# Kernel optimization log

Measured on AMD Instinct MI355X. Metric: run time of the kernel, lower is better.

The kernel has to match this reference:

```python
import jax, jax.numpy as jnp
import numpy as np

N, E, G, D, H = 50000, 800000, 64, 64, 256  # nodes, edges, graphs, feat dim, mlp hidden


def _mlp(x, W1, b1, W2, b2):
    return jax.nn.relu(x @ W1 + b1) @ W2 + b2


def _param(key, fan_in, fan_out):
    return jax.random.normal(key, (fan_in, fan_out), dtype=jnp.float32) * (1.0 / np.sqrt(fan_in))


def setup_inputs() -> dict:
    key = jax.random.key(0)
    ks = jax.random.split(key, 16)
    inp = {
        "nf": jax.random.normal(ks[0], (N, D), dtype=jnp.float32),
        "ef": jax.random.normal(ks[1], (E, D), dtype=jnp.float32),
        "u": jax.random.normal(ks[2], (G, D), dtype=jnp.float32),
        "src": jax.random.randint(ks[3], (E,), 0, N, dtype=jnp.int32),
        "dst": jax.random.randint(ks[4], (E,), 0, N, dtype=jnp.int32),
        "node_gid": jnp.sort(jax.random.randint(ks[5], (N,), 0, G, dtype=jnp.int32)),
        "edge_gid": jnp.sort(jax.random.randint(ks[6], (E,), 0, G, dtype=jnp.int32)),
        # edge_model: in = De + 2*Dn + Du = 4D
        "eW1": _param(ks[7], 4 * D, H), "eb1": jnp.zeros((H,), jnp.float32),
        "eW2": _param(ks[8], H, D),     "eb2": jnp.zeros((D,), jnp.float32),
        # node_model: in = De + Dn + Du = 3D
        "nW1": _param(ks[9], 3 * D, H), "nb1": jnp.zeros((H,), jnp.float32),
        "nW2": _param(ks[10], H, D),    "nb2": jnp.zeros((D,), jnp.float32),
        # global_model: in = De + Dn + Du = 3D
        "gW1": _param(ks[11], 3 * D, H), "gb1": jnp.zeros((H,), jnp.float32),
        "gW2": _param(ks[12], H, D),     "gb2": jnp.zeros((D,), jnp.float32),
    }
    return inp


def reference(nf, ef, u, src, dst, node_gid, edge_gid,
              eW1, eb1, eW2, eb2, nW1, nb1, nW2, nb2, gW1, gb1, gW2, gb2):
    # --- edge update: cat([ef, src_nf, dst_nf, u_per_edge]) -> edge MLP ---
    u_e = u[edge_gid]                                   # [E, D] (repeat_interleave by batch_num_edges)
    em_in = jnp.concatenate([ef, nf[src], nf[dst], u_e], axis=-1)  # [E, 4D]
    ef_new = _mlp(em_in, eW1, eb1, eW2, eb2)            # [E, D]

    # --- message = copy_e, reduce = sum at destination nodes ---
    agg_m = jax.ops.segment_sum(ef_new, dst, num_segments=N)       # [N, D]

    # --- node update: cat([agg_m, nf, u_per_node]) -> node MLP ---
    u_n = u[node_gid]                                   # [N, D]
    nm_in = jnp.concatenate([agg_m, nf, u_n], axis=-1)  # [N, 3D]
    nf_new = _mlp(nm_in, nW1, nb1, nW2, nb2)            # [N, D]

    # --- global update: per-graph sum readouts of updated edge/node feats ---
    e_aggr = jax.ops.segment_sum(ef_new, edge_gid, num_segments=G)  # [G, D]
    n_aggr = jax.ops.segment_sum(nf_new, node_gid, num_segments=G)  # [G, D]
    gm_in = jnp.concatenate([e_aggr, n_aggr, u], axis=-1)           # [G, 3D]
    u_new = _mlp(gm_in, gW1, gb1, gW2, gb2)             # [G, D]

    return nf_new, ef_new, u_new
```

## Files before the change

kernel.cpp:

```cpp
#include <hip/hip_runtime.h>
#include <stdint.h>
#include <stddef.h>

#define NN 50000
#define EE 800000
#define GG 64
#define DD 64
#define HH 256

typedef float f32x4 __attribute__((ext_vector_type(4)));
typedef short s16x8 __attribute__((ext_vector_type(8)));
typedef short s16x4 __attribute__((ext_vector_type(4)));

__device__ __forceinline__ short f2bf(float f) {
    union { float f; unsigned u; } v; v.f = f;
    return (short)((v.u + 0x7FFFu + ((v.u >> 16) & 1u)) >> 16);
}

__device__ __forceinline__ s16x4 f2bf4(f32x4 v) {
    s16x4 h = { f2bf(v.x), f2bf(v.y), f2bf(v.z), f2bf(v.w) };
    return h;
}

__global__ void prep_weights(const float* __restrict__ eW1, const float* __restrict__ eW2,
                             const float* __restrict__ nW1, const float* __restrict__ nW2,
                             short* __restrict__ W1t, short* __restrict__ W2t,
                             short* __restrict__ NW1t, short* __restrict__ NW2t) {
    int idx = blockIdx.x * blockDim.x + threadIdx.x;
    {
        int n = idx >> 8, k = idx & 255;
        W1t[idx] = f2bf(eW1[k * 256 + n]);
    }
    if (idx < 49152) {
        int n = idx / 192, k = idx - n * 192;
        NW1t[idx] = f2bf(nW1[k * 256 + n]);
    }
    if (idx < 16384) {
        int n = idx >> 8, k = idx & 255;
        W2t[idx]  = f2bf(eW2[k * 64 + n]);
        NW2t[idx] = f2bf(nW2[k * 64 + n]);
    }
}

#define SA1 264
#define SAN 200

__global__ __launch_bounds__(256, 2) void edge_kernel(
    const float* __restrict__ nf, const float* __restrict__ ef, const float* __restrict__ u,
    const int* __restrict__ src, const int* __restrict__ dst, const int* __restrict__ egid,
    const short* __restrict__ W1t, const float* __restrict__ b1,
    const short* __restrict__ W2t, const float* __restrict__ b2,
    float* __restrict__ ef_new, float* __restrict__ agg_m, float* __restrict__ e_aggr)
{
    __shared__ __align__(16) short As[64 * SA1];
    __shared__ __align__(16) short Y1s[64 * SA1];
    __shared__ int dstS[64];
    __shared__ int gidS[64];
    __shared__ float redS[4][64];

    const int t = threadIdx.x;
    const int wave = t >> 6, lane = t & 63;
    const int l15 = lane & 15, lq = lane >> 4;
    const int rsub = lane >> 4;
    const int c4l = (lane & 15) * 4;
    const int NB64 = gridDim.x * 64;

    const float* segbase = (wave == 0) ? ef : (wave == 3) ? u : nf;

    s16x8 w2f[8];
    {
        const short* bB2 = W2t + (size_t)(wave * 16 + l15) * 256 + lq * 8;
        #pragma unroll
        for (int kk = 0; kk < 8; ++kk) w2f[kk] = *(const s16x8*)(bB2 + kk * 32);
    }
    float bias1[4];
    #pragma unroll
    for (int ct = 0; ct < 4; ++ct) bias1[ct] = b1[wave * 64 + ct * 16 + l15];
    const float bo = b2[wave * 16 + l15];

    int e0 = blockIdx.x * 64;
    int idxc;
    f32x4 pf[16];
    if (wave == 0)      idxc = e0 + lane;
    else if (wave == 1) idxc = src[e0 + lane];
    else if (wave == 2) idxc = dst[e0 + lane];
    else                idxc = egid[e0 + lane];
    #pragma unroll
    for (int r = 0; r < 16; ++r) {
        int row = r * 4 + rsub;
        pf[r] = *(const f32x4*)(segbase + (size_t)__shfl(idxc, row) * 64 + c4l);
    }

    for (; e0 < EE; e0 += NB64) {
        const bool has_next = (e0 + NB64) < EE;

        #pragma unroll
        for (int r = 0; r < 16; ++r) {
            int row = r * 4 + rsub;
            *(s16x4*)(As + row * SA1 + wave * 64 + c4l) = f2bf4(pf[r]);
        }
        if (wave == 2)      dstS[lane] = idxc;
        else if (wave == 3) gidS[lane] = idxc;
        __syncthreads();

        int idxn;
        if (has_next) {
            int e0n = e0 + NB64;
            if (wave == 0)      idxn = e0n + lane;
            else if (wave == 1) idxn = src[e0n + lane];
            else if (wave == 2) idxn = dst[e0n + lane];
            else                idxn = egid[e0n + lane];
        }

        f32x4 acc[4][4] = {};
        {
            const short* aB = As + l15 * SA1 + lq * 8;
            const short* bB = W1t + (size_t)(wave * 64 + l15) * 256 + lq * 8;
            #pragma unroll
            for (int kk = 0; kk < 8; ++kk) {
                s16x8 a[4], b[4];
                #pragma unroll
                for (int rt = 0; rt < 4; ++rt) a[rt] = *(const s16x8*)(aB + rt * 16 * SA1 + kk * 32);
                #pragma unroll
                for (int ct = 0; ct < 4; ++ct) b[ct] = *(const s16x8*)(bB + (size_t)ct * 16 * 256 + kk * 32);
                #pragma unroll
                for (int rt = 0; rt < 4; ++rt)
                    #pragma unroll
                    for (int ct = 0; ct < 4; ++ct)
                        acc[rt][ct] = __builtin_amdgcn_mfma_f32_16x16x32_bf16(a[rt], b[ct], acc[rt][ct], 0, 0, 0);
            }
        }
        __syncthreads();

        #pragma unroll
        for (int ct = 0; ct < 4; ++ct) {
            int col = wave * 64 + ct * 16 + l15;
            float bb = bias1[ct];
            #pragma unroll
            for (int rt = 0; rt < 4; ++rt)
                #pragma unroll
                for (int r = 0; r < 4; ++r) {
                    int rr = rt * 16 + lq * 4 + r;
                    float v = acc[rt][ct][r] + bb;
                    Y1s[rr * SA1 + col] = f2bf(v > 0.f ? v : 0.f);
                }
        }

        if (has_next) {
            #pragma unroll
            for (int r = 0; r < 16; ++r) {
                int row = r * 4 + rsub;
                pf[r] = *(const f32x4*)(segbase + (size_t)__shfl(idxn, row) * 64 + c4l);
            }
        }
        __syncthreads();

        f32x4 acc2[4] = {};
        {
            const short* aB2 = Y1s + l15 * SA1 + lq * 8;
            #pragma unroll
            for (int kk = 0; kk < 8; ++kk) {
                #pragma unroll
                for (int rt = 0; rt < 4; ++rt) {
                    s16x8 a = *(const s16x8*)(aB2 + rt * 16 * SA1 + kk * 32);
                    acc2[rt] = __builtin_amdgcn_mfma_f32_16x16x32_bf16(a, w2f[kk], acc2[rt], 0, 0, 0);
                }
            }
        }
        __syncthreads();

        float* Y2s = (float*)Y1s;
        {
            const int colo = wave * 16 + l15;
            #pragma unroll
            for (int rt = 0; rt < 4; ++rt)
                #pragma unroll
                for (int r = 0; r < 4; ++r) {
                    int rr = rt * 16 + lq * 4 + r;
                    Y2s[rr * 65 + colo] = acc2[rt][r] + bo;
                }
        }
        __syncthreads();

        const bool uni = (gidS[0] == gidS[63]);
        const int g0 = gidS[0];
        float ps = 0.f;
        #pragma unroll
        for (int r = 0; r < 16; ++r) {
            int row = wave * 16 + r;
            float v = Y2s[row * 65 + lane];
            __builtin_nontemporal_store(v, &ef_new[(size_t)(e0 + row) * 64 + lane]);
            atomicAdd(&agg_m[(size_t)dstS[row] * 64 + lane], v);
            ps += v;
        }
        if (uni) redS[wave][lane] = ps;
        __syncthreads();

        if (uni) {
            if (wave == 0) {
                float s = redS[0][lane] + redS[1][lane] + redS[2][lane] + redS[3][lane];
                atomicAdd(&e_aggr[g0 * 64 + lane], s);
            }
        } else {
            if (t < 64) {
                float sum = 0.f; int g = gidS[0];
                for (int rr = 0; rr < 64; ++rr) {
                    int gg = gidS[rr];
                    if (gg != g) { atomicAdd(&e_aggr[g * 64 + t], sum); sum = 0.f; g = gg; }
                    sum += Y2s[rr * 65 + t];
                }
                atomicAdd(&e_aggr[g * 64 + t], sum);
            }
            __syncthreads();
        }

        if (has_next) idxc = idxn;
    }
}

__global__ __launch_bounds__(256, 4) void node_kernel(
    const float* __restrict__ nf, const float* __restrict__ u,
    const int* __restrict__ ngid, const float* __restrict__ agg_m,
    const short* __restrict__ W1t, const float* __restrict__ b1,
    const short* __restrict__ W2t, const float* __restrict__ b2,
    float* __restrict__ nf_new, float* __restrict__ n_aggr)
{
    __shared__ __align__(16) short As[64 * SA1];
    __shared__ int gidS[64];
    __shared__ float redS[4][64];

    const int t = threadIdx.x;
    const int n0 = blockIdx.x * 64;

    if (t < 64) gidS[t] = (n0 + t < NN) ? ngid[n0 + t] : -1;
    __syncthreads();

    #pragma unroll
    for (int itq = 0; itq < 4; ++itq) {
        int idx = itq * 256 + t;
        int row = idx >> 4;
        int c4 = (idx & 15) * 4;
        bool valid = (n0 + row) < NN;
        f32x4 va = {0.f, 0.f, 0.f, 0.f}, vb = va, vc = va;
        if (valid) {
            int g = gidS[row];
            va = *(const f32x4*)(agg_m + (size_t)(n0 + row) * 64 + c4);
            vb = *(const f32x4*)(nf + (size_t)(n0 + row) * 64 + c4);
            vc = *(const f32x4*)(u + (size_t)g * 64 + c4);
        }
        short* arow = As + row * SAN;
        *(s16x4*)(arow + c4)        = f2bf4(va);
        *(s16x4*)(arow + 64 + c4)   = f2bf4(vb);
        *(s16x4*)(arow + 128 + c4)  = f2bf4(vc);
    }
    __syncthreads();

    const int wave = t >> 6, lane = t & 63;
    const int l15 = lane & 15, lq = lane >> 4;

    f32x4 acc[4][4] = {};
    {
        const short* aB = As + l15 * SAN + lq * 8;
        const short* bB = W1t + (size_t)(wave * 64 + l15) * 192 + lq * 8;
        #pragma unroll
        for (int kk = 0; kk < 6; ++kk) {
            s16x8 a[4], b[4];
            #pragma unroll
            for (int rt = 0; rt < 4; ++rt) a[rt] = *(const s16x8*)(aB + rt * 16 * SAN + kk * 32);
            #pragma unroll
            for (int ct = 0; ct < 4; ++ct) b[ct] = *(const s16x8*)(bB + (size_t)ct * 16 * 192 + kk * 32);
            #pragma unroll
            for (int rt = 0; rt < 4; ++rt)
                #pragma unroll
                for (int ct = 0; ct < 4; ++ct)
                    acc[rt][ct] = __builtin_amdgcn_mfma_f32_16x16x32_bf16(a[rt], b[ct], acc[rt][ct], 0, 0, 0);
        }
    }
    __syncthreads();

    #pragma unroll
    for (int ct = 0; ct < 4; ++ct) {
        int col = wave * 64 + ct * 16 + l15;
        float bb = b1[col];
        #pragma unroll
        for (int rt = 0; rt < 4; ++rt)
            #pragma unroll
            for (int r = 0; r < 4; ++r) {
                int rr = rt * 16 + lq * 4 + r;
                float v = acc[rt][ct][r] + bb;
                As[rr * SA1 + col] = f2bf(v > 0.f ? v : 0.f);
            }
    }
    __syncthreads();

    f32x4 acc2[4] = {};
    {
        const short* aB2 = As + l15 * SA1 + lq * 8;
        const short* bB2 = W2t + (size_t)(wave * 16 + l15) * 256 + lq * 8;
        #pragma unroll
        for (int kk = 0; kk < 8; ++kk) {
            s16x8 b = *(const s16x8*)(bB2 + kk * 32);
            #pragma unroll
            for (int rt = 0; rt < 4; ++rt) {
                s16x8 a = *(const s16x8*)(aB2 + rt * 16 * SA1 + kk * 32);
                acc2[rt] = __builtin_amdgcn_mfma_f32_16x16x32_bf16(a, b, acc2[rt], 0, 0, 0);
            }
        }
    }
    __syncthreads();

    float* Y2s = (float*)As;
    {
        const int colo = wave * 16 + l15;
        const float bo = b2[colo];
        #pragma unroll
        for (int rt = 0; rt < 4; ++rt)
            #pragma unroll
            for (int r = 0; r < 4; ++r) {
                int rr = rt * 16 + lq * 4 + r;
                float v = acc2[rt][r] + bo;
                Y2s[rr * 65 + colo] = ((n0 + rr) < NN) ? v : 0.f;
            }
    }
    __syncthreads();

    const bool uni = (gidS[0] == gidS[63]) && (gidS[0] >= 0);
    const int g0 = gidS[0];
    float ps = 0.f;
    #pragma unroll
    for (int r = 0; r < 16; ++r) {
        int row = wave * 16 + r;
        float v = Y2s[row * 65 + lane];
        if ((n0 + row) < NN) nf_new[(size_t)(n0 + row) * 64 + lane] = v;
        ps += v;
    }
    if (uni) redS[wave][lane] = ps;
    __syncthreads();

    if (uni) {
        if (wave == 0) {
            float s = redS[0][lane] + redS[1][lane] + redS[2][lane] + redS[3][lane];
            atomicAdd(&n_aggr[g0 * 64 + lane], s);
        }
    } else if (t < 64) {
        float sum = 0.f; int g = gidS[0];
        for (int rr = 0; rr < 64; ++rr) {
            int gg = gidS[rr];
            if (gg != g) {
                if (g >= 0) atomicAdd(&n_aggr[g * 64 + t], sum);
                sum = 0.f; g = gg;
            }
            sum += Y2s[rr * 65 + t];
        }
        if (g >= 0) atomicAdd(&n_aggr[g * 64 + t], sum);
    }
}

__global__ void global_kernel(const float* __restrict__ e_aggr, const float* __restrict__ n_aggr,
                              const float* __restrict__ u,
                              const float* __restrict__ gW1, const float* __restrict__ gb1,
                              const float* __restrict__ gW2, const float* __restrict__ gb2,
                              float* __restrict__ u_new)
{
    __shared__ float gin[192];
    __shared__ float hid[256];
    const int g = blockIdx.x, t = threadIdx.x;
    if (t < 64)       gin[t] = e_aggr[g * 64 + t];
    else if (t < 128) gin[t] = n_aggr[g * 64 + (t - 64)];
    else if (t < 192) gin[t] = u[g * 64 + (t - 128)];
    __syncthreads();
    float s = gb1[t];
    #pragma unroll 8
    for (int k = 0; k < 192; ++k) s += gin[k] * gW1[k * 256 + t];
    hid[t] = s > 0.f ? s : 0.f;
    __syncthreads();
    if (t < 64) {
        float o = gb2[t];
        #pragma unroll 8
        for (int k = 0; k < 256; ++k) o += hid[k] * gW2[k * 64 + t];
        u_new[g * 64 + t] = o;
    }
}

#define WS_AGGM_OFF   0u
#define WS_AGGM_BYTES (NN * 64u * 4u)
#define WS_EAGG_OFF   (WS_AGGM_OFF + WS_AGGM_BYTES)
#define WS_NAGG_OFF   (WS_EAGG_OFF + GG * 64u * 4u)
#define WS_ZERO_BYTES (WS_NAGG_OFF + GG * 64u * 4u)
#define WS_W1T_OFF    WS_ZERO_BYTES
#define WS_W2T_OFF    (WS_W1T_OFF + 65536u * 2u)
#define WS_NW1T_OFF   (WS_W2T_OFF + 16384u * 2u)
#define WS_NW2T_OFF   (WS_NW1T_OFF + 49152u * 2u)

extern "C" void kernel_launch(void* const* d_in, const int* in_sizes, int n_in,
                              void* d_out, int out_size, void* d_ws, size_t ws_size,
                              hipStream_t stream) {
    const float* nf  = (const float*)d_in[0];
    const float* ef  = (const float*)d_in[1];
    const float* u   = (const float*)d_in[2];
    const int* src   = (const int*)d_in[3];
    const int* dst   = (const int*)d_in[4];
    const int* ngid  = (const int*)d_in[5];
    const int* egid  = (const int*)d_in[6];
    const float* eW1 = (const float*)d_in[7];
    const float* eb1 = (const float*)d_in[8];
    const float* eW2 = (const float*)d_in[9];
    const float* eb2 = (const float*)d_in[10];
    const float* nW1 = (const float*)d_in[11];
    const float* nb1 = (const float*)d_in[12];
    const float* nW2 = (const float*)d_in[13];
    const float* nb2 = (const float*)d_in[14];
    const float* gW1 = (const float*)d_in[15];
    const float* gb1 = (const float*)d_in[16];
    const float* gW2 = (const float*)d_in[17];
    const float* gb2 = (const float*)d_in[18];

    float* out    = (float*)d_out;
    float* nf_new = out;
    float* ef_new = out + (size_t)NN * DD;
    float* u_new  = out + (size_t)(NN + EE) * DD;

    char* ws = (char*)d_ws;
    float* agg_m  = (float*)(ws + WS_AGGM_OFF);
    float* e_aggr = (float*)(ws + WS_EAGG_OFF);
    float* n_aggr = (float*)(ws + WS_NAGG_OFF);
    short* W1t    = (short*)(ws + WS_W1T_OFF);
    short* W2t    = (short*)(ws + WS_W2T_OFF);
    short* NW1t   = (short*)(ws + WS_NW1T_OFF);
    short* NW2t   = (short*)(ws + WS_NW2T_OFF);

    hipMemsetAsync(d_ws, 0, WS_ZERO_BYTES, stream);
    prep_weights<<<256, 256, 0, stream>>>(eW1, eW2, nW1, nW2, W1t, W2t, NW1t, NW2t);
    edge_kernel<<<512, 256, 0, stream>>>(nf, ef, u, src, dst, egid,
                                         W1t, eb1, W2t, eb2, ef_new, agg_m, e_aggr);
    node_kernel<<<(NN + 63) / 64, 256, 0, stream>>>(nf, u, ngid, agg_m,
                                                    NW1t, nb1, NW2t, nb2, nf_new, n_aggr);
    global_kernel<<<GG, 256, 0, stream>>>(e_aggr, n_aggr, u, gW1, gb1, gW2, gb2, u_new);
}
```

Measured before the change: 758.6 us.

## Replace scatter atomics with CSR gather for destination aggregation

```diff
diff --git a/kernel.cpp b/kernel.cpp
--- a/kernel.cpp
+++ b/kernel.cpp
@@ -42,185 +42,187 @@
     }
 }
 
+__global__ void hist_kernel(const int* __restrict__ dst, int* __restrict__ deg) {
+    int e = blockIdx.x * blockDim.x + threadIdx.x;
+    if (e < EE) atomicAdd(&deg[dst[e]], 1);
+}
+
+__global__ __launch_bounds__(1024) void scan_kernel(const int* __restrict__ deg,
+                                                    int* __restrict__ rowptr,
+                                                    int* __restrict__ cursor) {
+    __shared__ int part[1024];
+    const int t = threadIdx.x;
+    const int CH = 49;
+    int loc[CH];
+    int s = 0;
+    #pragma unroll
+    for (int i = 0; i < CH; ++i) {
+        int idx = t * CH + i;
+        loc[i] = s;
+        s += (idx < NN) ? deg[idx] : 0;
+    }
+    part[t] = s;
+    __syncthreads();
+    const int own = s;
+    for (int off = 1; off < 1024; off <<= 1) {
+        int v = (t >= off) ? part[t - off] : 0;
+        __syncthreads();
+        part[t] += v;
+        __syncthreads();
+    }
+    const int excl = part[t] - own;
+    #pragma unroll
+    for (int i = 0; i < CH; ++i) {
+        int idx = t * CH + i;
+        if (idx < NN) { int v = excl + loc[i]; rowptr[idx] = v; cursor[idx] = v; }
+    }
+    if (t == 0) rowptr[NN] = EE;
+}
+
+__global__ void fill_kernel(const int* __restrict__ dst, int* __restrict__ cursor,
+                            int* __restrict__ eidx) {
+    int e = blockIdx.x * blockDim.x + threadIdx.x;
+    if (e < EE) {
+        int d = dst[e];
+        int pos = atomicAdd(&cursor[d], 1);
+        eidx[pos] = e;
+    }
+}
+
 #define SA1 264
 #define SAN 200
 
-__global__ __launch_bounds__(256, 2) void edge_kernel(
+__global__ __launch_bounds__(256, 4) void edge_kernel(
     const float* __restrict__ nf, const float* __restrict__ ef, const float* __restrict__ u,
     const int* __restrict__ src, const int* __restrict__ dst, const int* __restrict__ egid,
     const short* __restrict__ W1t, const float* __restrict__ b1,
     const short* __restrict__ W2t, const float* __restrict__ b2,
-    float* __restrict__ ef_new, float* __restrict__ agg_m, float* __restrict__ e_aggr)
+    float* __restrict__ ef_new, float* __restrict__ e_aggr)
 {
     __shared__ __align__(16) short As[64 * SA1];
-    __shared__ __align__(16) short Y1s[64 * SA1];
-    __shared__ int dstS[64];
     __shared__ int gidS[64];
     __shared__ float redS[4][64];
 
     const int t = threadIdx.x;
+    const int e0 = blockIdx.x * 64;
     const int wave = t >> 6, lane = t & 63;
     const int l15 = lane & 15, lq = lane >> 4;
-    const int rsub = lane >> 4;
-    const int c4l = (lane & 15) * 4;
-    const int NB64 = gridDim.x * 64;
+
+    int idxv;
+    if (wave == 0)      idxv = e0 + lane;
+    else if (wave == 1) idxv = src[e0 + lane];
+    else if (wave == 2) idxv = dst[e0 + lane];
+    else                { idxv = egid[e0 + lane]; gidS[lane] = idxv; }
 
     const float* segbase = (wave == 0) ? ef : (wave == 3) ? u : nf;
 
-    s16x8 w2f[8];
-    {
-        const short* bB2 = W2t + (size_t)(wave * 16 + l15) * 256 + lq * 8;
-        #pragma unroll
-        for (int kk = 0; kk < 8; ++kk) w2f[kk] = *(const s16x8*)(bB2 + kk * 32);
-    }
-    float bias1[4];
-    #pragma unroll
-    for (int ct = 0; ct < 4; ++ct) bias1[ct] = b1[wave * 64 + ct * 16 + l15];
-    const float bo = b2[wave * 16 + l15];
-
-    int e0 = blockIdx.x * 64;
-    int idxc;
-    f32x4 pf[16];
-    if (wave == 0)      idxc = e0 + lane;
-    else if (wave == 1) idxc = src[e0 + lane];
-    else if (wave == 2) idxc = dst[e0 + lane];
-    else                idxc = egid[e0 + lane];
+    {
+        const int rsub = lane >> 4;
+        const int c4 = (lane & 15) * 4;
+        #pragma unroll
+        for (int r = 0; r < 16; ++r) {
+            const int row = r * 4 + rsub;
+            const float* sp = segbase + (size_t)__shfl(idxv, row) * 64 + c4;
+            f32x4 v = *(const f32x4*)sp;
+            *(s16x4*)(As + row * SA1 + wave * 64 + c4) = f2bf4(v);
+        }
+    }
+    __syncthreads();
+
+    f32x4 acc[4][4] = {};
+    const short* aB = As + l15 * SA1 + lq * 8;
+    const short* bB = W1t + (size_t)(wave * 64 + l15) * 256 + lq * 8;
+    #pragma unroll
+    for (int kk = 0; kk < 8; ++kk) {
+        s16x8 a[4], b[4];
+        #pragma unroll
+        for (int rt = 0; rt < 4; ++rt) a[rt] = *(const s16x8*)(aB + rt * 16 * SA1 + kk * 32);
+        #pragma unroll
+        for (int ct = 0; ct < 4; ++ct) b[ct] = *(const s16x8*)(bB + (size_t)ct * 16 * 256 + kk * 32);
+        #pragma unroll
+        for (int rt = 0; rt < 4; ++rt)
+            #pragma unroll
+            for (int ct = 0; ct < 4; ++ct)
+                acc[rt][ct] = __builtin_amdgcn_mfma_f32_16x16x32_bf16(a[rt], b[ct], acc[rt][ct], 0, 0, 0);
+    }
+    __syncthreads();
+
+    #pragma unroll
+    for (int ct = 0; ct < 4; ++ct) {
+        int col = wave * 64 + ct * 16 + l15;
+        float bb = b1[col];
+        #pragma unroll
+        for (int rt = 0; rt < 4; ++rt)
+            #pragma unroll
+            for (int r = 0; r < 4; ++r) {
+                int rr = rt * 16 + lq * 4 + r;
+                float v = acc[rt][ct][r] + bb;
+                As[rr * SA1 + col] = f2bf(v > 0.f ? v : 0.f);
+            }
+    }
+    __syncthreads();
+
+    f32x4 acc2[4] = {};
+    const short* aB2 = As + l15 * SA1 + lq * 8;
+    const short* bB2 = W2t + (size_t)(wave * 16 + l15) * 256 + lq * 8;
+    #pragma unroll
+    for (int kk = 0; kk < 8; ++kk) {
+        s16x8 b = *(const s16x8*)(bB2 + kk * 32);
+        #pragma unroll
+        for (int rt = 0; rt < 4; ++rt) {
+            s16x8 a = *(const s16x8*)(aB2 + rt * 16 * SA1 + kk * 32);
+            acc2[rt] = __builtin_amdgcn_mfma_f32_16x16x32_bf16(a, b, acc2[rt], 0, 0, 0);
+        }
+    }
+    __syncthreads();
+
+    float* Y2s = (float*)As;
+    {
+        const int colo = wave * 16 + l15;
+        const float bo = b2[colo];
+        #pragma unroll
+        for (int rt = 0; rt < 4; ++rt)
+            #pragma unroll
+            for (int r = 0; r < 4; ++r) {
+                int rr = rt * 16 + lq * 4 + r;
+                Y2s[rr * 65 + colo] = acc2[rt][r] + bo;
+            }
+    }
+    __syncthreads();
+
+    const bool uni = (gidS[0] == gidS[63]);
+    const int g0 = gidS[0];
+    float ps = 0.f;
     #pragma unroll
     for (int r = 0; r < 16; ++r) {
-        int row = r * 4 + rsub;
-        pf[r] = *(const f32x4*)(segbase + (size_t)__shfl(idxc, row) * 64 + c4l);
-    }
-
-    for (; e0 < EE; e0 += NB64) {
-        const bool has_next = (e0 + NB64) < EE;
-
-        #pragma unroll
-        for (int r = 0; r < 16; ++r) {
-            int row = r * 4 + rsub;
-            *(s16x4*)(As + row * SA1 + wave * 64 + c4l) = f2bf4(pf[r]);
-        }
-        if (wave == 2)      dstS[lane] = idxc;
-        else if (wave == 3) gidS[lane] = idxc;
-        __syncthreads();
-
-        int idxn;
-        if (has_next) {
-            int e0n = e0 + NB64;
-            if (wave == 0)      idxn = e0n + lane;
-            else if (wave == 1) idxn = src[e0n + lane];
-            else if (wave == 2) idxn = dst[e0n + lane];
-            else                idxn = egid[e0n + lane];
-        }
-
-        f32x4 acc[4][4] = {};
-        {
-            const short* aB = As + l15 * SA1 + lq * 8;
-            const short* bB = W1t + (size_t)(wave * 64 + l15) * 256 + lq * 8;
-            #pragma unroll
-            for (int kk = 0; kk < 8; ++kk) {
-                s16x8 a[4], b[4];
-                #pragma unroll
-                for (int rt = 0; rt < 4; ++rt) a[rt] = *(const s16x8*)(aB + rt * 16 * SA1 + kk * 32);
-                #pragma unroll
-                for (int ct = 0; ct < 4; ++ct) b[ct] = *(const s16x8*)(bB + (size_t)ct * 16 * 256 + kk * 32);
-                #pragma unroll
-                for (int rt = 0; rt < 4; ++rt)
-                    #pragma unroll
-                    for (int ct = 0; ct < 4; ++ct)
-                        acc[rt][ct] = __builtin_amdgcn_mfma_f32_16x16x32_bf16(a[rt], b[ct], acc[rt][ct], 0, 0, 0);
-            }
-        }
-        __syncthreads();
-
-        #pragma unroll
-        for (int ct = 0; ct < 4; ++ct) {
-            int col = wave * 64 + ct * 16 + l15;
-            float bb = bias1[ct];
-            #pragma unroll
-            for (int rt = 0; rt < 4; ++rt)
-                #pragma unroll
-                for (int r = 0; r < 4; ++r) {
-                    int rr = rt * 16 + lq * 4 + r;
-                    float v = acc[rt][ct][r] + bb;
-                    Y1s[rr * SA1 + col] = f2bf(v > 0.f ? v : 0.f);
-                }
-        }
-
-        if (has_next) {
-            #pragma unroll
-            for (int r = 0; r < 16; ++r) {
-                int row = r * 4 + rsub;
-                pf[r] = *(const f32x4*)(segbase + (size_t)__shfl(idxn, row) * 64 + c4l);
-            }
-        }
-        __syncthreads();
-
-        f32x4 acc2[4] = {};
-        {
-            const short* aB2 = Y1s + l15 * SA1 + lq * 8;
-            #pragma unroll
-            for (int kk = 0; kk < 8; ++kk) {
-                #pragma unroll
-                for (int rt = 0; rt < 4; ++rt) {
-                    s16x8 a = *(const s16x8*)(aB2 + rt * 16 * SA1 + kk * 32);
-                    acc2[rt] = __builtin_amdgcn_mfma_f32_16x16x32_bf16(a, w2f[kk], acc2[rt], 0, 0, 0);
-                }
-            }
-        }
-        __syncthreads();
-
-        float* Y2s = (float*)Y1s;
-        {
-            const int colo = wave * 16 + l15;
-            #pragma unroll
-            for (int rt = 0; rt < 4; ++rt)
-                #pragma unroll
-                for (int r = 0; r < 4; ++r) {
-                    int rr = rt * 16 + lq * 4 + r;
-                    Y2s[rr * 65 + colo] = acc2[rt][r] + bo;
-                }
-        }
-        __syncthreads();
-
-        const bool uni = (gidS[0] == gidS[63]);
-        const int g0 = gidS[0];
-        float ps = 0.f;
-        #pragma unroll
-        for (int r = 0; r < 16; ++r) {
-            int row = wave * 16 + r;
-            float v = Y2s[row * 65 + lane];
-            __builtin_nontemporal_store(v, &ef_new[(size_t)(e0 + row) * 64 + lane]);
-            atomicAdd(&agg_m[(size_t)dstS[row] * 64 + lane], v);
-            ps += v;
-        }
-        if (uni) redS[wave][lane] = ps;
-        __syncthreads();
-
-        if (uni) {
-            if (wave == 0) {
-                float s = redS[0][lane] + redS[1][lane] + redS[2][lane] + redS[3][lane];
-                atomicAdd(&e_aggr[g0 * 64 + lane], s);
-            }
-        } else {
-            if (t < 64) {
-                float sum = 0.f; int g = gidS[0];
-                for (int rr = 0; rr < 64; ++rr) {
-                    int gg = gidS[rr];
-                    if (gg != g) { atomicAdd(&e_aggr[g * 64 + t], sum); sum = 0.f; g = gg; }
-                    sum += Y2s[rr * 65 + t];
-                }
-                atomicAdd(&e_aggr[g * 64 + t], sum);
-            }
-            __syncthreads();
-        }
-
-        if (has_next) idxc = idxn;
+        int row = wave * 16 + r;
+        float v = Y2s[row * 65 + lane];
+        ef_new[(size_t)(e0 + row) * 64 + lane] = v;
+        ps += v;
+    }
+    if (uni) redS[wave][lane] = ps;
+    __syncthreads();
+
+    if (uni) {
+        if (wave == 0) {
+            float s = redS[0][lane] + redS[1][lane] + redS[2][lane] + redS[3][lane];
+            atomicAdd(&e_aggr[g0 * 64 + lane], s);
+        }
+    } else if (t < 64) {
+        float sum = 0.f; int g = gidS[0];
+        for (int rr = 0; rr < 64; ++rr) {
+            int gg = gidS[rr];
+            if (gg != g) { atomicAdd(&e_aggr[g * 64 + t], sum); sum = 0.f; g = gg; }
+            sum += Y2s[rr * 65 + t];
+        }
+        atomicAdd(&e_aggr[g * 64 + t], sum);
     }
 }
 
 __global__ __launch_bounds__(256, 4) void node_kernel(
     const float* __restrict__ nf, const float* __restrict__ u,
-    const int* __restrict__ ngid, const float* __restrict__ agg_m,
+    const int* __restrict__ ngid, const float* __restrict__ ef_new,
+    const int* __restrict__ rowptr, const int* __restrict__ eidx,
     const short* __restrict__ W1t, const float* __restrict__ b1,
     const short* __restrict__ W2t, const float* __restrict__ b2,
     float* __restrict__ nf_new, float* __restrict__ n_aggr)
@@ -241,17 +243,34 @@
         int row = idx >> 4;
         int c4 = (idx & 15) * 4;
         bool valid = (n0 + row) < NN;
-        f32x4 va = {0.f, 0.f, 0.f, 0.f}, vb = va, vc = va;
+        f32x4 vb = {0.f, 0.f, 0.f, 0.f}, vc = vb;
         if (valid) {
             int g = gidS[row];
-            va = *(const f32x4*)(agg_m + (size_t)(n0 + row) * 64 + c4);
             vb = *(const f32x4*)(nf + (size_t)(n0 + row) * 64 + c4);
             vc = *(const f32x4*)(u + (size_t)g * 64 + c4);
         }
         short* arow = As + row * SAN;
-        *(s16x4*)(arow + c4)        = f2bf4(va);
         *(s16x4*)(arow + 64 + c4)   = f2bf4(vb);
         *(s16x4*)(arow + 128 + c4)  = f2bf4(vc);
+    }
+
+    {
+        const int grp = t >> 4;
+        const int sl = t & 15;
+        for (int b = 0; b < 4; ++b) {
+            int row = b * 16 + grp;
+            int node = n0 + row;
+            f32x4 acc = {0.f, 0.f, 0.f, 0.f};
+            if (node < NN) {
+                int p0 = rowptr[node], p1 = rowptr[node + 1];
+                for (int p = p0; p < p1; ++p) {
+                    int e = eidx[p];
+                    f32x4 v = *(const f32x4*)(ef_new + (size_t)e * 64 + sl * 4);
+                    acc.x += v.x; acc.y += v.y; acc.z += v.z; acc.w += v.w;
+                }
+            }
+            *(s16x4*)(As + row * SAN + sl * 4) = f2bf4(acc);
+        }
     }
     __syncthreads();
 
@@ -382,12 +401,14 @@
     }
 }
 
-#define WS_AGGM_OFF   0u
-#define WS_AGGM_BYTES (NN * 64u * 4u)
-#define WS_EAGG_OFF   (WS_AGGM_OFF + WS_AGGM_BYTES)
-#define WS_NAGG_OFF   (WS_EAGG_OFF + GG * 64u * 4u)
-#define WS_ZERO_BYTES (WS_NAGG_OFF + GG * 64u * 4u)
-#define WS_W1T_OFF    WS_ZERO_BYTES
+#define WS_DEG_OFF    0u
+#define WS_EAGG_OFF   200000u
+#define WS_NAGG_OFF   216384u
+#define WS_ZERO_BYTES 232768u
+#define WS_ROWPTR_OFF 232768u
+#define WS_CURSOR_OFF (WS_ROWPTR_OFF + 200016u)
+#define WS_EIDX_OFF   (WS_CURSOR_OFF + 200016u)
+#define WS_W1T_OFF    (WS_EIDX_OFF + 3200000u)
 #define WS_W2T_OFF    (WS_W1T_OFF + 65536u * 2u)
 #define WS_NW1T_OFF   (WS_W2T_OFF + 16384u * 2u)
 #define WS_NW2T_OFF   (WS_NW1T_OFF + 49152u * 2u)
@@ -421,19 +442,25 @@
     float* u_new  = out + (size_t)(NN + EE) * DD;
 
     char* ws = (char*)d_ws;
-    float* agg_m  = (float*)(ws + WS_AGGM_OFF);
+    int* deg     = (int*)(ws + WS_DEG_OFF);
     float* e_aggr = (float*)(ws + WS_EAGG_OFF);
     float* n_aggr = (float*)(ws + WS_NAGG_OFF);
-    short* W1t    = (short*)(ws + WS_W1T_OFF);
-    short* W2t    = (short*)(ws + WS_W2T_OFF);
-    short* NW1t   = (short*)(ws + WS_NW1T_OFF);
-    short* NW2t   = (short*)(ws + WS_NW2T_OFF);
+    int* rowptr  = (int*)(ws + WS_ROWPTR_OFF);
+    int* cursor  = (int*)(ws + WS_CURSOR_OFF);
+    int* eidx    = (int*)(ws + WS_EIDX_OFF);
+    short* W1t   = (short*)(ws + WS_W1T_OFF);
+    short* W2t   = (short*)(ws + WS_W2T_OFF);
+    short* NW1t  = (short*)(ws + WS_NW1T_OFF);
+    short* NW2t  = (short*)(ws + WS_NW2T_OFF);
 
     hipMemsetAsync(d_ws, 0, WS_ZERO_BYTES, stream);
     prep_weights<<<256, 256, 0, stream>>>(eW1, eW2, nW1, nW2, W1t, W2t, NW1t, NW2t);
-    edge_kernel<<<512, 256, 0, stream>>>(nf, ef, u, src, dst, egid,
-                                         W1t, eb1, W2t, eb2, ef_new, agg_m, e_aggr);
-    node_kernel<<<(NN + 63) / 64, 256, 0, stream>>>(nf, u, ngid, agg_m,
+    hist_kernel<<<EE / 256, 256, 0, stream>>>(dst, deg);
+    scan_kernel<<<1, 1024, 0, stream>>>(deg, rowptr, cursor);
+    fill_kernel<<<EE / 256, 256, 0, stream>>>(dst, cursor, eidx);
+    edge_kernel<<<EE / 64, 256, 0, stream>>>(nf, ef, u, src, dst, egid,
+                                             W1t, eb1, W2t, eb2, ef_new, e_aggr);
+    node_kernel<<<(NN + 63) / 64, 256, 0, stream>>>(nf, u, ngid, ef_new, rowptr, eidx,
                                                     NW1t, nb1, NW2t, nb2, nf_new, n_aggr);
     global_kernel<<<GG, 256, 0, stream>>>(e_aggr, n_aggr, u, gW1, gb1, gW2, gb2, u_new);
 }
```

Result: slower. 921.5 us (+21.5%).
